# Performance work log

Hardware: AMD Instinct MI355X
Metric: run time of the kernel (lower is better)

## Reference

```python
import jax, jax.numpy as jnp
import numpy as np

DIM = 768      # d_model
D_INNER = 768  # int(ssm_ratio * dim)
KK = 16        # K (scan groups)
CD = 48        # Cdim per group (hardcoded self.C)
NS = 16        # d_state
BATCH, SEQ = 8, 4096


def setup_inputs() -> dict:
    key = jax.random.key(0)
    ks = jax.random.split(key, 12)
    s_in = (2.0 / (DIM + 2 * D_INNER)) ** 0.5   # ~xavier
    s_out = (2.0 / (D_INNER + DIM)) ** 0.5
    return {
        "x": jax.random.normal(ks[0], (BATCH, SEQ, DIM), jnp.float32),
        "in_proj_w": jax.random.normal(ks[1], (2 * D_INNER, DIM), jnp.float32) * s_in,
        "in_proj_b": jnp.zeros((2 * D_INNER,), jnp.float32),
        "conv_w": jax.random.normal(ks[2], (D_INNER, 1, 3, 3), jnp.float32) * 0.2,
        "conv_b": jnp.zeros((D_INNER,), jnp.float32),
        "out_proj_w": jax.random.normal(ks[3], (DIM, D_INNER), jnp.float32) * s_out,
        "out_proj_b": jnp.zeros((DIM,), jnp.float32),
        "A_logs": jax.random.normal(ks[4], (KK * CD, NS), jnp.float32) * 0.1,
        "delta": jax.random.normal(ks[5], (BATCH, KK * CD, SEQ), jnp.float32),
        "B_t": jax.random.normal(ks[6], (BATCH, KK, NS, SEQ), jnp.float32),
        "C_t": jax.random.normal(ks[7], (BATCH, KK, NS, SEQ), jnp.float32),
        "delta_bias": jax.random.normal(ks[8], (KK * CD,), jnp.float32),
    }


def reference(x, in_proj_w, in_proj_b, conv_w, conv_b, out_proj_w, out_proj_b,
              A_logs, delta, B_t, C_t, delta_bias):
    # in_proj + chunk; z = silu(z) in the original is dead code (never used)
    h = x @ in_proj_w.T + in_proj_b                      # (B,N,2*D)
    u = h[..., :D_INNER]                                  # (B,N,D)
    # depthwise 3x3 conv on a (B,D,N,1) map (width-1 input, pad 1)
    u = u.transpose(0, 2, 1)[..., None]                   # (B,D,N,1)
    u = jax.lax.conv_general_dilated(
        u, conv_w, window_strides=(1, 1), padding=((1, 1), (1, 1)),
        dimension_numbers=("NCHW", "OIHW", "NCHW"),
        feature_group_count=D_INNER)
    u = jax.nn.silu(u[..., 0] + conv_b[None, :, None])    # (B,D,N)

    # selective_scan_torch math (note: NOT a true recurrence in the source):
    #   delta <- softplus(delta + delta_bias)
    #   y[b,d,l] = delta^2 * u * sum_n A[d,n] * B[b,k(d),n,l] * C[b,k(d),n,l]
    d = jax.nn.softplus(delta + delta_bias[None, :, None])  # (B,D,L)
    A = A_logs.reshape(KK, CD, NS)
    s = jnp.einsum("kcn,bknl->bkcl", A, B_t * C_t)           # (B,K,Cd,L)
    s = s.reshape(u.shape[0], D_INNER, u.shape[2])           # (B,D,L)
    y = d * d * u * s                                        # (B,D,L)

    out = y.transpose(0, 2, 1) @ out_proj_w.T + out_proj_b   # (B,N,dim)
    return out
```

## Files before the change

kernel.cpp:

```cpp
#include <hip/hip_runtime.h>
#include <math.h>

#define B_  8
#define S_  4096
#define D_  768
#define K_  16
#define C_  48
#define N_  16
#define M_  (B_*S_)

typedef float  f32x4  __attribute__((ext_vector_type(4)));
typedef __bf16 bf16x8 __attribute__((ext_vector_type(8)));

__device__ __forceinline__ ushort f2bf(float f) {
  uint u = __builtin_bit_cast(uint, f);
  u += 0x7FFFu + ((u >> 16) & 1u);
  return (ushort)(u >> 16);
}
__device__ __forceinline__ float bf2f(ushort h) {
  return __builtin_bit_cast(float, (uint)h << 16);
}

__global__ __launch_bounds__(256)
void cvt_f32_bf16(const float* __restrict__ in, ushort* __restrict__ out, int n4) {
  const int stride = gridDim.x * 256;
  for (int i = blockIdx.x * 256 + threadIdx.x; i < n4; i += stride) {
    float4 v = *reinterpret_cast<const float4*>(in + (size_t)i * 4);
    ushort4 o;
    o.x = f2bf(v.x); o.y = f2bf(v.y); o.z = f2bf(v.z); o.w = f2bf(v.w);
    *reinterpret_cast<ushort4*>(out + (size_t)i * 4) = o;
  }
}

template<bool OUT_BF16>
__global__ __launch_bounds__(256)
void gemm_mfma_bt(const ushort* __restrict__ A, const ushort* __restrict__ Bm,
                  const float* __restrict__ bias, void* __restrict__ Cc)
{
  __shared__ ushort As[128 * 32];
  __shared__ ushort Bs[128 * 32];

  const int lin = blockIdx.x;
  const int swz = (lin & 7) * 192 + (lin >> 3);
  const int bn  = (swz % 6) * 128;
  const int bm  = (swz / 6) * 128;

  const int tid  = threadIdx.x;
  const int wid  = tid >> 6, lane = tid & 63;
  const int wr   = wid >> 1, wc   = wid & 1;
  const int lr   = lane & 15, lg  = lane >> 4;
  const int srow = lane >> 2;
  const int scol = (lane & 3) * 8;

  f32x4 acc[4][4];
#pragma unroll
  for (int i = 0; i < 4; ++i)
#pragma unroll
    for (int j = 0; j < 4; ++j) acc[i][j] = (f32x4){0.f, 0.f, 0.f, 0.f};

  for (int k0 = 0; k0 < 768; k0 += 32) {
#pragma unroll
    for (int jj = 0; jj < 2; ++jj) {
      const int j = wid * 2 + jj;
      const ushort* ga = A  + (size_t)(bm + j * 16 + srow) * 768 + k0 + scol;
      __builtin_amdgcn_global_load_lds(
          (const __attribute__((address_space(1))) void*)ga,
          (__attribute__((address_space(3))) void*)(As + j * 512), 16, 0, 0);
      const ushort* gb = Bm + (size_t)(bn + j * 16 + srow) * 768 + k0 + scol;
      __builtin_amdgcn_global_load_lds(
          (const __attribute__((address_space(1))) void*)gb,
          (__attribute__((address_space(3))) void*)(Bs + j * 512), 16, 0, 0);
    }
    __syncthreads();

    bf16x8 af[4], bfr[4];
    const int ab = (wr * 64 + lr) * 32 + lg * 8;
    const int bb = (wc * 64 + lr) * 32 + lg * 8;
#pragma unroll
    for (int mf = 0; mf < 4; ++mf) af[mf]  = *reinterpret_cast<const bf16x8*>(&As[ab + mf * 512]);
#pragma unroll
    for (int nf = 0; nf < 4; ++nf) bfr[nf] = *reinterpret_cast<const bf16x8*>(&Bs[bb + nf * 512]);
#pragma unroll
    for (int mf = 0; mf < 4; ++mf)
#pragma unroll
      for (int nf = 0; nf < 4; ++nf)
        acc[mf][nf] = __builtin_amdgcn_mfma_f32_16x16x32_bf16(af[mf], bfr[nf], acc[mf][nf], 0, 0, 0);
    __syncthreads();
  }

#pragma unroll
  for (int nf = 0; nf < 4; ++nf) {
    const int n  = bn + wc * 64 + nf * 16 + lr;
    const float bv = bias[n];
#pragma unroll
    for (int mf = 0; mf < 4; ++mf) {
      const int m0 = bm + wr * 64 + mf * 16 + lg * 4;
#pragma unroll
      for (int r = 0; r < 4; ++r) {
        const float v = acc[mf][nf][r] + bv;
        if (OUT_BF16) ((ushort*)Cc)[(size_t)(m0 + r) * 768 + n] = f2bf(v);
        else          ((float*) Cc)[(size_t)(m0 + r) * 768 + n] = v;
      }
    }
  }
}

#define U0P 68
#define YSP 70

__global__ __launch_bounds__(256)
void fuse_mid(const ushort* __restrict__ u0b, const float* __restrict__ delta,
              const float* __restrict__ Bt, const float* __restrict__ Ct,
              const float* __restrict__ Alog, const float* __restrict__ convw,
              const float* __restrict__ convb, const float* __restrict__ dbias,
              ushort* __restrict__ yT)
{
  __shared__ float  Gs [N_ * 64];
  __shared__ float  Ak [C_ * N_];
  __shared__ ushort U0T[C_ * U0P];
  __shared__ ushort Ys [C_ * YSP];
  __shared__ float  Wk0[C_], Wk1[C_], Wk2[C_], CB[C_], DB[C_];

  const int tid = threadIdx.x;
  const int wid = tid >> 6, lane = tid & 63;
  const int lt = blockIdx.x, k = blockIdx.y, b = blockIdx.z;
  const int l0 = lt * 64;

  for (int idx = tid; idx < N_ * 64; idx += 256) {
    const int n = idx >> 6, dl = idx & 63;
    const size_t g = (((size_t)b * K_ + k) * N_ + n) * S_ + l0 + dl;
    Gs[idx] = Bt[g] * Ct[g];
  }
  for (int idx = tid; idx < C_ * N_; idx += 256)
    Ak[idx] = Alog[(size_t)k * C_ * N_ + idx];
  if (tid < C_) {
    Wk0[tid] = convw[(k * C_ + tid) * 9 + 1];
    Wk1[tid] = convw[(k * C_ + tid) * 9 + 4];
    Wk2[tid] = convw[(k * C_ + tid) * 9 + 7];
    CB [tid] = convb[k * C_ + tid];
    DB [tid] = dbias[k * C_ + tid];
  }
  {
    const uint* usrc = reinterpret_cast<const uint*>(u0b);
    for (int idx = tid; idx < 66 * 24; idx += 256) {
      const int l = idx / 24, j = idx - l * 24;
      const int gl = l0 + l - 1;
      uint v = 0;
      if (gl >= 0 && gl < S_) v = usrc[(size_t)((size_t)b * S_ + gl) * 384 + k * 24 + j];
      U0T[(2 * j    ) * U0P + l] = (ushort)(v & 0xffffu);
      U0T[(2 * j + 1) * U0P + l] = (ushort)(v >> 16);
    }
  }
  __syncthreads();

  float g[N_];
#pragma unroll
  for (int n = 0; n < N_; ++n) g[n] = Gs[n * 64 + lane];

  for (int step = 0; step < 12; ++step) {
    const int c = step * 4 + wid;
    float a[N_];
#pragma unroll
    for (int n4 = 0; n4 < 4; ++n4)
      *reinterpret_cast<f32x4*>(&a[n4 * 4]) =
          *reinterpret_cast<const f32x4*>(&Ak[c * N_ + n4 * 4]);

    const float dv = delta[((size_t)b * D_ + k * C_ + c) * S_ + l0 + lane] + DB[c];
    const float d  = (dv > 15.f) ? dv : __logf(1.f + __expf(dv));

    float x = fmaf(Wk0[c], bf2f(U0T[c * U0P + lane]),
              fmaf(Wk1[c], bf2f(U0T[c * U0P + lane + 1]),
              fmaf(Wk2[c], bf2f(U0T[c * U0P + lane + 2]), CB[c])));
    const float u = x * __builtin_amdgcn_rcpf(1.f + __expf(-x));

    float s = 0.f;
#pragma unroll
    for (int n = 0; n < N_; ++n) s = fmaf(a[n], g[n], s);

    Ys[c * YSP + lane] = f2bf(d * d * u * s);
  }
  __syncthreads();

  for (int e = tid; e < C_ * 64; e += 256) {
    const int c = e % C_, dl = e / C_;
    yT[((size_t)((size_t)b * S_ + l0 + dl)) * D_ + k * C_ + c] = Ys[c * YSP + dl];
  }
}

extern "C" void kernel_launch(void* const* d_in, const int* in_sizes, int n_in,
                              void* d_out, int out_size, void* d_ws, size_t ws_size,
                              hipStream_t stream) {
  const float* x      = (const float*)d_in[0];
  const float* in_w   = (const float*)d_in[1];
  const float* in_b   = (const float*)d_in[2];
  const float* convw  = (const float*)d_in[3];
  const float* convb  = (const float*)d_in[4];
  const float* out_w  = (const float*)d_in[5];
  const float* out_b  = (const float*)d_in[6];
  const float* Alog   = (const float*)d_in[7];
  const float* delta  = (const float*)d_in[8];
  const float* Bt     = (const float*)d_in[9];
  const float* Ct     = (const float*)d_in[10];
  const float* dbias  = (const float*)d_in[11];
  float* out = (float*)d_out;

  ushort* xb  = (ushort*)d_ws;
  ushort* u0b = xb  + (size_t)M_ * D_;
  ushort* yTb = u0b + (size_t)M_ * D_;
  ushort* wb1 = yTb + (size_t)M_ * D_;
  ushort* wb2 = wb1 + (size_t)D_ * D_;

  cvt_f32_bf16<<<2048, 256, 0, stream>>>(x,     xb,  M_ * D_ / 4);
  cvt_f32_bf16<<<576,  256, 0, stream>>>(in_w,  wb1, D_ * D_ / 4);
  cvt_f32_bf16<<<576,  256, 0, stream>>>(out_w, wb2, D_ * D_ / 4);

  gemm_mfma_bt<true ><<<1536, 256, 0, stream>>>(xb, wb1, in_b, u0b);
  fuse_mid<<<dim3(S_ / 64, K_, B_), 256, 0, stream>>>(u0b, delta, Bt, Ct, Alog, convw, convb, dbias, yTb);
  gemm_mfma_bt<false><<<1536, 256, 0, stream>>>(yTb, wb2, out_b, out);
}
```

Baseline: 230.2 us.

## Merge conversion launches, prefetch delta, pad U0T, strength-reduce index math

Folds the three f32-to-bf16 conversion kernels into one launch that splits work by block index, which saves two kernel launches. In fuse_mid, the delta loads are software-prefetched two steps ahead to hide global latency. The U0T LDS row pitch changes to an odd value to reduce bank conflicts on the transposed stores. Division and modulo in the staging and writeback loops are replaced with incremental index updates. These are small independent tweaks, and the extra prefetch registers could cost some occupancy.

```diff
diff --git a/kernel.cpp b/kernel.cpp
--- a/kernel.cpp
+++ b/kernel.cpp
@@ -22,9 +22,16 @@
 }
 
 __global__ __launch_bounds__(256)
-void cvt_f32_bf16(const float* __restrict__ in, ushort* __restrict__ out, int n4) {
-  const int stride = gridDim.x * 256;
-  for (int i = blockIdx.x * 256 + threadIdx.x; i < n4; i += stride) {
+void cvt_all(const float* __restrict__ x, const float* __restrict__ w1,
+             const float* __restrict__ w2, ushort* __restrict__ xb,
+             ushort* __restrict__ wb1, ushort* __restrict__ wb2) {
+  const int b = blockIdx.x;
+  const float* in; ushort* out; int n4, nb, b0;
+  if (b < 2048)      { in = x;  out = xb;  n4 = M_ * D_ / 4; nb = 2048; b0 = 0; }
+  else if (b < 2624) { in = w1; out = wb1; n4 = D_ * D_ / 4; nb = 576;  b0 = 2048; }
+  else               { in = w2; out = wb2; n4 = D_ * D_ / 4; nb = 576;  b0 = 2624; }
+  const int stride = nb * 256;
+  for (int i = (b - b0) * 256 + threadIdx.x; i < n4; i += stride) {
     float4 v = *reinterpret_cast<const float4*>(in + (size_t)i * 4);
     ushort4 o;
     o.x = f2bf(v.x); o.y = f2bf(v.y); o.z = f2bf(v.z); o.w = f2bf(v.w);
@@ -105,7 +112,7 @@
   }
 }
 
-#define U0P 68
+#define U0P 67
 #define YSP 70
 
 __global__ __launch_bounds__(256)
@@ -128,8 +135,8 @@
 
   for (int idx = tid; idx < N_ * 64; idx += 256) {
     const int n = idx >> 6, dl = idx & 63;
-    const size_t g = (((size_t)b * K_ + k) * N_ + n) * S_ + l0 + dl;
-    Gs[idx] = Bt[g] * Ct[g];
+    const size_t gg = (((size_t)b * K_ + k) * N_ + n) * S_ + l0 + dl;
+    Gs[idx] = Bt[gg] * Ct[gg];
   }
   for (int idx = tid; idx < C_ * N_; idx += 256)
     Ak[idx] = Alog[(size_t)k * C_ * N_ + idx];
@@ -142,13 +149,14 @@
   }
   {
     const uint* usrc = reinterpret_cast<const uint*>(u0b);
+    int l = tid / 24, j = tid - (tid / 24) * 24;
     for (int idx = tid; idx < 66 * 24; idx += 256) {
-      const int l = idx / 24, j = idx - l * 24;
       const int gl = l0 + l - 1;
       uint v = 0;
-      if (gl >= 0 && gl < S_) v = usrc[(size_t)((size_t)b * S_ + gl) * 384 + k * 24 + j];
+      if (gl >= 0 && gl < S_) v = usrc[((size_t)b * S_ + gl) * 384 + k * 24 + j];
       U0T[(2 * j    ) * U0P + l] = (ushort)(v & 0xffffu);
       U0T[(2 * j + 1) * U0P + l] = (ushort)(v >> 16);
+      l += 10; j += 16; if (j >= 24) { j -= 24; l += 1; }
     }
   }
   __syncthreads();
@@ -156,22 +164,31 @@
   float g[N_];
 #pragma unroll
   for (int n = 0; n < N_; ++n) g[n] = Gs[n * 64 + lane];
+
+  const float* dp = delta + ((size_t)b * D_ + k * C_ + wid) * S_ + l0 + lane;
+  const size_t dstr = (size_t)4 * S_;
+  float dn0 = dp[0];
+  float dn1 = dp[dstr];
 
   for (int step = 0; step < 12; ++step) {
     const int c = step * 4 + wid;
+    const float dcur = dn0;
+    dn0 = dn1;
+    dn1 = (step < 10) ? dp[(size_t)(step + 2) * dstr] : 0.f;
+
     float a[N_];
 #pragma unroll
-    for (int n4 = 0; n4 < 4; ++n4)
-      *reinterpret_cast<f32x4*>(&a[n4 * 4]) =
-          *reinterpret_cast<const f32x4*>(&Ak[c * N_ + n4 * 4]);
-
-    const float dv = delta[((size_t)b * D_ + k * C_ + c) * S_ + l0 + lane] + DB[c];
+    for (int n4i = 0; n4i < 4; ++n4i)
+      *reinterpret_cast<f32x4*>(&a[n4i * 4]) =
+          *reinterpret_cast<const f32x4*>(&Ak[c * N_ + n4i * 4]);
+
+    const float dv = dcur + DB[c];
     const float d  = (dv > 15.f) ? dv : __logf(1.f + __expf(dv));
 
-    float x = fmaf(Wk0[c], bf2f(U0T[c * U0P + lane]),
-              fmaf(Wk1[c], bf2f(U0T[c * U0P + lane + 1]),
-              fmaf(Wk2[c], bf2f(U0T[c * U0P + lane + 2]), CB[c])));
-    const float u = x * __builtin_amdgcn_rcpf(1.f + __expf(-x));
+    float xx = fmaf(Wk0[c], bf2f(U0T[c * U0P + lane]),
+               fmaf(Wk1[c], bf2f(U0T[c * U0P + lane + 1]),
+               fmaf(Wk2[c], bf2f(U0T[c * U0P + lane + 2]), CB[c])));
+    const float u = xx * __builtin_amdgcn_rcpf(1.f + __expf(-xx));
 
     float s = 0.f;
 #pragma unroll
@@ -181,9 +198,12 @@
   }
   __syncthreads();
 
-  for (int e = tid; e < C_ * 64; e += 256) {
-    const int c = e % C_, dl = e / C_;
-    yT[((size_t)((size_t)b * S_ + l0 + dl)) * D_ + k * C_ + c] = Ys[c * YSP + dl];
+  {
+    int dl = tid / 48, c = tid - (tid / 48) * 48;
+    for (int e = tid; e < C_ * 64; e += 256) {
+      yT[((size_t)b * S_ + l0 + dl) * D_ + k * C_ + c] = Ys[c * YSP + dl];
+      dl += 5; c += 16; if (c >= 48) { c -= 48; dl += 1; }
+    }
   }
 }
 
@@ -210,9 +230,7 @@
   ushort* wb1 = yTb + (size_t)M_ * D_;
   ushort* wb2 = wb1 + (size_t)D_ * D_;
 
-  cvt_f32_bf16<<<2048, 256, 0, stream>>>(x,     xb,  M_ * D_ / 4);
-  cvt_f32_bf16<<<576,  256, 0, stream>>>(in_w,  wb1, D_ * D_ / 4);
-  cvt_f32_bf16<<<576,  256, 0, stream>>>(out_w, wb2, D_ * D_ / 4);
+  cvt_all<<<3200, 256, 0, stream>>>(x, in_w, out_w, xb, wb1, wb2);
 
   gemm_mfma_bt<true ><<<1536, 256, 0, stream>>>(xb, wb1, in_b, u0b);
   fuse_mid<<<dim3(S_ / 64, K_, B_), 256, 0, stream>>>(u0b, delta, Bt, Ct, Alog, convw, convb, dbias, yTb);
```

Result: no change. 228.1 us (-0.9%).
